# Performance work log

Hardware: AMD Instinct MI355X
Metric: run time of the kernel (lower is better)

## Reference

```python
import jax, jax.numpy as jnp
import numpy as np

B, E, CIN, C, PRE, DME, DEN = 8, 64, 128, 128, 128, 32, 32
N_EDGE_TYPES, N_PATH_TYPES = 10, 20


def leaky(v):
    return jnp.where(v >= 0, v, 0.1 * v)


def setup_inputs() -> dict:
    key = jax.random.key(0)
    ks = jax.random.split(key, 30)
    s = 0.05
    inp = {
        'x': jax.random.normal(ks[0], (B, CIN, E), jnp.float32),
        'y': jax.random.normal(ks[1], (B, CIN, E), jnp.float32),
        'm_bias_mat': jax.random.normal(ks[2], (B, E, E), jnp.float32),
        'edge_mat': jax.random.randint(ks[3], (B, E, E), 0, N_EDGE_TYPES),
        'p_bias_mat': jax.random.normal(ks[4], (B, E, E, E), jnp.float32),
        'path_mat': jax.random.randint(ks[5], (B, E, E, E), 0, N_PATH_TYPES),
        'pre_out': jax.random.normal(ks[6], (B, PRE, E, E), jnp.float32),
        # parameters (conv1d/conv2d k=1 weights squeezed to matrices/vectors)
        'xc1_w': jax.random.normal(ks[7], (C, CIN), jnp.float32) * s,
        'yc1_w': jax.random.normal(ks[8], (C, CIN), jnp.float32) * s,
        'xc2_w': jax.random.normal(ks[9], (C,), jnp.float32) * s,
        'xc2_b': jax.random.normal(ks[10], (1,), jnp.float32) * s,
        'yc2_w': jax.random.normal(ks[11], (C,), jnp.float32) * s,
        'yc2_b': jax.random.normal(ks[12], (1,), jnp.float32) * s,
        'pconv_w': jax.random.normal(ks[13], (DEN,), jnp.float32) * s,
        'econv_w': jax.random.normal(ks[14], (DME,), jnp.float32) * s,
        'conv1_w': jax.random.normal(ks[15], (C, 2 * C + PRE), jnp.float32) * s,
        'conv1_b': jax.random.normal(ks[16], (C,), jnp.float32) * s,
        'conv2_w': jax.random.normal(ks[17], (C, C, 3, 3), jnp.float32) * s,
        'conv2_b': jax.random.normal(ks[18], (C,), jnp.float32) * s,
        'score_w': jax.random.normal(ks[19], (C,), jnp.float32) * s,
        'xlin_w': jax.random.normal(ks[20], (CIN, CIN), jnp.float32) * s,
        'ylin_w': jax.random.normal(ks[21], (CIN, CIN), jnp.float32) * s,
        'edge_table': jax.random.normal(ks[22], (N_EDGE_TYPES, DME), jnp.float32) * s,
        'path_table': jax.random.normal(ks[23], (N_PATH_TYPES, DEN), jnp.float32) * s,
    }
    return inp


def reference(x, y, m_bias_mat, edge_mat, p_bias_mat, path_mat, pre_out,
              xc1_w, yc1_w, xc2_w, xc2_b, yc2_w, yc2_b, pconv_w, econv_w,
              conv1_w, conv1_b, conv2_w, conv2_b, score_w, xlin_w, ylin_w,
              edge_table, path_table):
    # x,y: [B, CIN, E]; M == N == entity_num == E (required by path_fea reshape)
    x_f = jnp.einsum('ci,bim->bcm', xc1_w, x)                    # [B,C,M]
    y_f = jnp.einsum('ci,bin->bcn', yc1_w, y)                    # [B,C,N]
    x_self = jnp.einsum('c,bcm->bm', xc2_w, x_f) + xc2_b         # [B,M]
    y_other = jnp.einsum('c,bcn->bn', yc2_w, y_f) + yc2_b        # [B,N]
    # torch broadcast: [B,1,M] + [B,N,1] -> [B,N,M]
    logist = leaky(x_self[:, None, :] + y_other[:, :, None])     # [B,E,E]

    # ---- per-entity path attention (vectorized over entity axis e) ----
    path_embed = path_table[path_mat]                            # [B,E,M,N,DEN]
    path_logist = leaky(jnp.einsum('bemnd,d->bemn', path_embed, pconv_w))
    local = logist[:, None, :, :] + path_logist + p_bias_mat     # [B,E,M,N]
    A = jax.nn.softmax(local, axis=-1)
    x_ret = leaky(jnp.einsum('bemn,bcn->bcem', A, y_f) + x_f[:, :, None, :])  # [B,C,E,M]
    A2 = jax.nn.softmax(jnp.swapaxes(local, 2, 3), axis=-1)
    y_ret = leaky(jnp.einsum('benm,bcm->bcen', A2, x_f) + y_f[:, :, None, :])  # [B,C,E,N]
    path_fea = jnp.concatenate([x_ret, y_ret], axis=1)           # [B,2C,E,E]

    men = jnp.concatenate([path_fea, pre_out], axis=1)           # [B,2C+PRE,E,E]
    h = leaky(jnp.einsum('oc,bcij->boij', conv1_w, men) + conv1_b[None, :, None, None])
    h = jax.lax.conv_general_dilated(h, conv2_w, (1, 1), 'SAME',
                                     dimension_numbers=('NCHW', 'OIHW', 'NCHW'))
    men2rel = leaky(h + conv2_b[None, :, None, None])            # [B,C,E,E]

    scores = leaky(jnp.einsum('c,bcij->bij', score_w, men2rel))  # [B,E,E]
    edge_logist = leaky(jnp.einsum('bmnd,d->bmn', edge_table[edge_mat], econv_w))
    g = logist + scores + edge_logist + m_bias_mat               # [B,E,E]

    x_lin = jnp.einsum('ij,bjm->bmi', xlin_w, x)                 # [B,M,CIN]
    y_lin = jnp.einsum('ij,bjn->bni', ylin_w, y)                 # [B,N,CIN]
    G = jax.nn.softmax(g, axis=-1)
    out_x = jnp.einsum('bmn,bni->bim', G, y_lin) + x             # residual, [B,CIN,M]
    G2 = jax.nn.softmax(jnp.swapaxes(g, 1, 2), axis=-1)
    out_y = jnp.einsum('bnm,bmi->bin', G2, x_lin) + y            # [B,CIN,N]
    return (out_x, out_y, men2rel)
```

## Files before the change

### kernel.cpp

```cpp
#include <hip/hip_runtime.h>
#include <hip/hip_bf16.h>


typedef unsigned short u16;
typedef unsigned int u32;
typedef short s16x8 __attribute__((ext_vector_type(8)));
typedef float f32x4 __attribute__((ext_vector_type(4)));

__device__ __forceinline__ float b2f(u16 u) { return __uint_as_float(((u32)u) << 16); }
__device__ __forceinline__ u16 f2b(float f) {
    u32 x = __float_as_uint(f);
    u32 r = (x + 0x7fffu + ((x >> 16) & 1u)) >> 16;
    return (u16)r;
}
__device__ __forceinline__ float lk(float v) { return v >= 0.f ? v : 0.1f * v; }
__device__ __forceinline__ s16x8 cvt8(const float* p) {
    float4 a = ((const float4*)p)[0], c = ((const float4*)p)[1];
    s16x8 r;
    r[0] = (short)f2b(a.x); r[1] = (short)f2b(a.y); r[2] = (short)f2b(a.z); r[3] = (short)f2b(a.w);
    r[4] = (short)f2b(c.x); r[5] = (short)f2b(c.y); r[6] = (short)f2b(c.z); r[7] = (short)f2b(c.w);
    return r;
}

__global__ __launch_bounds__(256) void k_prep(const float* __restrict__ w1, const float* __restrict__ w2,
                                              u16* __restrict__ wA1, u16* __restrict__ wA2,
                                              const float* __restrict__ x, const float* __restrict__ y,
                                              const float* __restrict__ xc1, const float* __restrict__ yc1,
                                              const float* __restrict__ xc2w, const float* __restrict__ xc2b,
                                              const float* __restrict__ yc2w, const float* __restrict__ yc2b,
                                              const float* __restrict__ xlw, const float* __restrict__ ylw,
                                              u16* __restrict__ xfb, u16* __restrict__ yfb,
                                              float* __restrict__ xfT, float* __restrict__ yfT,
                                              u16* __restrict__ xlT, u16* __restrict__ ylT,
                                              float* __restrict__ Xs, float* __restrict__ Yo,
                                              const float* __restrict__ pre, u16* __restrict__ menT) {
    int bid = blockIdx.x;
    int t = threadIdx.x;
    if (bid < 768) {
        int idx = bid * 256 + t;
        if (idx < 49152) {
            int e = idx & 7, lane = (idx >> 3) & 63, mtg = (idx >> 9) & 7, kc = idx >> 12;
            int o = mtg * 16 + (lane & 15), c = kc * 32 + ((lane >> 4) << 3) + e;
            wA1[idx] = f2b(w1[o * 384 + c]);
        } else {
            int id2 = idx - 49152;
            if (id2 < 147456) {
                int e = id2 & 7, lane = (id2 >> 3) & 63, mtg = (id2 >> 9) & 7;
                int kc = (id2 >> 12) & 3, tap = id2 >> 14;
                int o = mtg * 16 + (lane & 15), c = kc * 32 + ((lane >> 4) << 3) + e;
                wA2[id2] = f2b(w2[(o * 128 + c) * 9 + tap]);
            }
        }
        return;
    }
    if (bid < 800) {
        int r = bid - 768;
        int b = r >> 2, g4 = r & 3;
        int lane = t & 63, w = t >> 6, l15 = lane & 15, q4 = lane >> 4;
        __shared__ u16 sT[64][136];
        const float* src = (g4 == 0 || g4 == 2) ? x : y;
        const float* wptr = (g4 == 0) ? xc1 : (g4 == 1) ? yc1 : (g4 == 2) ? xlw : ylw;
        {
            int i = t >> 1, m0 = (t & 1) * 32;
            const float4* ps = (const float4*)(src + (b * 128 + i) * 64 + m0);
#pragma unroll
            for (int q = 0; q < 8; ++q) {
                float4 v = ps[q];
                int m = m0 + q * 4;
                sT[m + 0][i] = f2b(v.x); sT[m + 1][i] = f2b(v.y);
                sT[m + 2][i] = f2b(v.z); sT[m + 3][i] = f2b(v.w);
            }
        }
        __syncthreads();
        int m = w * 16 + l15;
        f32x4 acc[8];
#pragma unroll
        for (int mt = 0; mt < 8; ++mt) acc[mt] = (f32x4)(0.f);
#pragma unroll
        for (int kt = 0; kt < 4; ++kt) {
            s16x8 bfr = *(const s16x8*)&sT[m][kt * 32 + q4 * 8];
#pragma unroll
            for (int mt = 0; mt < 8; ++mt) {
                s16x8 af = cvt8(wptr + (mt * 16 + l15) * 128 + kt * 32 + q4 * 8);
                acc[mt] = __builtin_amdgcn_mfma_f32_16x16x32_bf16(af, bfr, acc[mt], 0, 0, 0);
            }
        }
        if (g4 == 0 || g4 == 1) {
            u16* fb = (g4 == 0) ? xfb : yfb;
            float* fT = (g4 == 0) ? xfT : yfT;
            const float* c2w = (g4 == 0) ? xc2w : yc2w;
            const float* c2b = (g4 == 0) ? xc2b : yc2b;
            float* dvec = (g4 == 0) ? Xs : Yo;
            float sp = 0.f;
#pragma unroll
            for (int mt = 0; mt < 8; ++mt) {
                int c0 = mt * 16 + q4 * 4;
                f32x4 a = acc[mt];
                fb[(b * 128 + c0 + 0) * 64 + m] = f2b(a[0]);
                fb[(b * 128 + c0 + 1) * 64 + m] = f2b(a[1]);
                fb[(b * 128 + c0 + 2) * 64 + m] = f2b(a[2]);
                fb[(b * 128 + c0 + 3) * 64 + m] = f2b(a[3]);
                *(float4*)(fT + (b * 64 + m) * 128 + c0) = make_float4(a[0], a[1], a[2], a[3]);
                float4 wv = *(const float4*)(c2w + c0);
                sp += wv.x * a[0] + wv.y * a[1] + wv.z * a[2] + wv.w * a[3];
            }
            sp += __shfl_xor(sp, 16);
            sp += __shfl_xor(sp, 32);
            if (q4 == 0) dvec[b * 64 + m] = sp + c2b[0];
        } else {
            u16* lT = (g4 == 2) ? xlT : ylT;
#pragma unroll
            for (int mt = 0; mt < 8; ++mt) {
                int i0 = mt * 16 + q4 * 4;
                f32x4 a = acc[mt];
                lT[(b * 128 + i0 + 0) * 64 + m] = f2b(a[0]);
                lT[(b * 128 + i0 + 1) * 64 + m] = f2b(a[1]);
                lT[(b * 128 + i0 + 2) * 64 + m] = f2b(a[2]);
                lT[(b * 128 + i0 + 3) * 64 + m] = f2b(a[3]);
            }
        }
        return;
    }
    {
        int r = bid - 800;
        int b = r >> 6, i = r & 63;
        int j = t & 63, pg = t >> 6;
#pragma unroll
        for (int oc = 0; oc < 4; ++oc) {
            int p0 = pg * 32 + oc * 8;
            s16x8 v;
#pragma unroll
            for (int k = 0; k < 8; ++k)
                v[k] = (short)f2b(pre[((b * 128 + p0 + k) * 64 + i) * 64 + j]);
            *(s16x8*)(menT + ((b * 64 + i) * 64 + j) * 384 + 256 + p0) = v;
        }
    }
}

__global__ __launch_bounds__(256) void k_attn(const float* __restrict__ Xs, const float* __restrict__ Yo,
                                              const u16* __restrict__ xfb, const u16* __restrict__ yfb,
                                              const float* __restrict__ xfT, const float* __restrict__ yfT,
                                              const int* __restrict__ path_mat, const float* __restrict__ p_bias,
                                              const float* __restrict__ ptab, const float* __restrict__ pconv,
                                              u16* __restrict__ menT) {
    int b = blockIdx.x >> 6, e = blockIdx.x & 63;
    int t = threadIdx.x;
    int lane = t & 63, w = t >> 6;
    __shared__ float sA[64][68];
    __shared__ u16 Abf[64][72];
    __shared__ u16 E2bf[64][72];
    __shared__ float sRed[256];
    __shared__ float sPdot[20];
    __shared__ float sXv[64], sYv[64];

    if (t < 20) {
        float s = 0.f;
        for (int d = 0; d < 32; ++d) s += ptab[t * 32 + d] * pconv[d];
        sPdot[t] = lk(s);
    } else if (t >= 64 && t < 128) {
        sXv[t - 64] = Xs[b * 64 + t - 64];
    } else if (t >= 128 && t < 192) {
        sYv[t - 128] = Yo[b * 64 + t - 128];
    }
    __syncthreads();

    {
        int m = t >> 2, n0 = (t & 3) * 16;
        int base = (((b * 64 + e) * 64 + m) * 64 + n0);
        const int4* pm4 = (const int4*)(path_mat + base);
        const float4* pb4 = (const float4*)(p_bias + base);
        float yom = sYv[m];
#pragma unroll
        for (int q = 0; q < 4; ++q) {
            int4 pm = pm4[q]; float4 pb = pb4[q];
            int n = n0 + q * 4;
            float4 v;
            v.x = lk(sXv[n + 0] + yom) + sPdot[pm.x] + pb.x;
            v.y = lk(sXv[n + 1] + yom) + sPdot[pm.y] + pb.y;
            v.z = lk(sXv[n + 2] + yom) + sPdot[pm.z] + pb.z;
            v.w = lk(sXv[n + 3] + yom) + sPdot[pm.w] + pb.w;
            *(float4*)&sA[m][n] = v;
        }
    }
    __syncthreads();

    if (t < 128) {
        int r = t >> 1, h = t & 1;
        const float4* rp = (const float4*)&sA[r][h * 32];
        float mx = -1e30f;
#pragma unroll
        for (int k = 0; k < 8; ++k) {
            float4 v = rp[k];
            mx = fmaxf(mx, fmaxf(fmaxf(v.x, v.y), fmaxf(v.z, v.w)));
        }
        mx = fmaxf(mx, __shfl_xor(mx, 1));
        float s = 0.f;
#pragma unroll
        for (int k = 0; k < 8; ++k) {
            float4 v = rp[k];
            s += __expf(v.x - mx) + __expf(v.y - mx) + __expf(v.z - mx) + __expf(v.w - mx);
        }
        s += __shfl_xor(s, 1);
        if (h == 0) { sRed[r] = mx; sRed[64 + r] = 1.f / s; }
    } else {
        int n = (t - 128) >> 1, h = t & 1;
        float mx = -1e30f;
#pragma unroll
        for (int k = 0; k < 32; ++k) mx = fmaxf(mx, sA[h * 32 + k][n]);
        mx = fmaxf(mx, __shfl_xor(mx, 1));
        float s = 0.f;
#pragma unroll
        for (int k = 0; k < 32; ++k) s += __expf(sA[h * 32 + k][n] - mx);
        s += __shfl_xor(s, 1);
        if (h == 0) { sRed[128 + n] = mx; sRed[192 + n] = 1.f / s; }
    }
    __syncthreads();

    {
        int m = t >> 2, q = t & 3;
        float rmax = sRed[m], rinv = sRed[64 + m];
        const float4* rp = (const float4*)&sA[m][q * 16];
#pragma unroll
        for (int g2 = 0; g2 < 2; ++g2) {
            float4 v0 = rp[g2 * 2], v1 = rp[g2 * 2 + 1];
            s16x8 pk;
            pk[0] = (short)f2b(__expf(v0.x - rmax) * rinv);
            pk[1] = (short)f2b(__expf(v0.y - rmax) * rinv);
            pk[2] = (short)f2b(__expf(v0.z - rmax) * rinv);
            pk[3] = (short)f2b(__expf(v0.w - rmax) * rinv);
            pk[4] = (short)f2b(__expf(v1.x - rmax) * rinv);
            pk[5] = (short)f2b(__expf(v1.y - rmax) * rinv);
            pk[6] = (short)f2b(__expf(v1.z - rmax) * rinv);
            pk[7] = (short)f2b(__expf(v1.w - rmax) * rinv);
            *(s16x8*)&Abf[m][q * 16 + g2 * 8] = pk;
        }
    }
    {
        int n = t >> 2, q = t & 3;
        float cmax = sRed[128 + n], cinv = sRed[192 + n];
#pragma unroll
        for (int g2 = 0; g2 < 2; ++g2) {
            s16x8 pk;
#pragma unroll
            for (int k = 0; k < 8; ++k) {
                float v = sA[q * 16 + g2 * 8 + k][n];
                pk[k] = (short)f2b(__expf(v - cmax) * cinv);
            }
            *(s16x8*)&E2bf[n][q * 16 + g2 * 8] = pk;
        }
    }
    __syncthreads();

    int l15 = lane & 15, q4 = lane >> 4;
    {
        f32x4 acc[2][4];
#pragma unroll
        for (int ci = 0; ci < 2; ++ci)
#pragma unroll
            for (int mt = 0; mt < 4; ++mt) acc[ci][mt] = (f32x4)(0.f);
#pragma unroll
        for (int kt = 0; kt < 2; ++kt) {
            s16x8 afr[2];
#pragma unroll
            for (int ci = 0; ci < 2; ++ci) {
                int c = (2 * w + ci) * 16 + l15;
                afr[ci] = *(const s16x8*)(yfb + (b * 128 + c) * 64 + kt * 32 + q4 * 8);
            }
            s16x8 bfr[4];
#pragma unroll
            for (int mt = 0; mt < 4; ++mt)
                bfr[mt] = *(const s16x8*)&Abf[mt * 16 + l15][kt * 32 + q4 * 8];
#pragma unroll
            for (int ci = 0; ci < 2; ++ci)
#pragma unroll
                for (int mt = 0; mt < 4; ++mt)
                    acc[ci][mt] = __builtin_amdgcn_mfma_f32_16x16x32_bf16(afr[ci], bfr[mt], acc[ci][mt], 0, 0, 0);
        }
#pragma unroll
        for (int ci = 0; ci < 2; ++ci) {
            int c0 = (2 * w + ci) * 16 + q4 * 4;
#pragma unroll
            for (int mt = 0; mt < 4; ++mt) {
                int m = mt * 16 + l15;
                float4 res = *(const float4*)(xfT + (b * 64 + m) * 128 + c0);
                f32x4 a = acc[ci][mt];
                u32 lo = (u32)f2b(lk(a[0] + res.x)) | ((u32)f2b(lk(a[1] + res.y)) << 16);
                u32 hi = (u32)f2b(lk(a[2] + res.z)) | ((u32)f2b(lk(a[3] + res.w)) << 16);
                *(uint2*)(menT + ((b * 64 + e) * 64 + m) * 384 + c0) = make_uint2(lo, hi);
            }
        }
    }
    {
        f32x4 acc[2][4];
#pragma unroll
        for (int ci = 0; ci < 2; ++ci)
#pragma unroll
            for (int nt = 0; nt < 4; ++nt) acc[ci][nt] = (f32x4)(0.f);
#pragma unroll
        for (int kt = 0; kt < 2; ++kt) {
            s16x8 afr[2];
#pragma unroll
            for (int ci = 0; ci < 2; ++ci) {
                int c = (2 * w + ci) * 16 + l15;
                afr[ci] = *(const s16x8*)(xfb + (b * 128 + c) * 64 + kt * 32 + q4 * 8);
            }
            s16x8 bfr[4];
#pragma unroll
            for (int nt = 0; nt < 4; ++nt)
                bfr[nt] = *(const s16x8*)&E2bf[nt * 16 + l15][kt * 32 + q4 * 8];
#pragma unroll
            for (int ci = 0; ci < 2; ++ci)
#pragma unroll
                for (int nt = 0; nt < 4; ++nt)
                    acc[ci][nt] = __builtin_amdgcn_mfma_f32_16x16x32_bf16(afr[ci], bfr[nt], acc[ci][nt], 0, 0, 0);
        }
#pragma unroll
        for (int ci = 0; ci < 2; ++ci) {
            int c0 = (2 * w + ci) * 16 + q4 * 4;
#pragma unroll
            for (int nt = 0; nt < 4; ++nt) {
                int n = nt * 16 + l15;
                float4 res = *(const float4*)(yfT + (b * 64 + n) * 128 + c0);
                f32x4 a = acc[ci][nt];
                u32 lo = (u32)f2b(lk(a[0] + res.x)) | ((u32)f2b(lk(a[1] + res.y)) << 16);
                u32 hi = (u32)f2b(lk(a[2] + res.z)) | ((u32)f2b(lk(a[3] + res.w)) << 16);
                *(uint2*)(menT + ((b * 64 + e) * 64 + n) * 384 + 128 + c0) = make_uint2(lo, hi);
            }
        }
    }
}

__global__ __launch_bounds__(256) void k_conv1(const u16* __restrict__ menT, const u16* __restrict__ wA1,
                                               const float* __restrict__ b1, u16* __restrict__ hT) {
    int b = blockIdx.x >> 6, i = blockIdx.x & 63;
    int t = threadIdx.x;
    int lane = t & 63, w = t >> 6, wm = w & 1, wn = w >> 1;
    int l15 = lane & 15, q4 = lane >> 4;

    f32x4 acc[4][2];
#pragma unroll
    for (int mt = 0; mt < 4; ++mt)
#pragma unroll
        for (int nt = 0; nt < 2; ++nt) acc[mt][nt] = (f32x4)(0.f);

    const u16* mrow = menT + (b * 64 + i) * 64 * 384;
    for (int kc = 0; kc < 12; ++kc) {
        s16x8 af[4];
#pragma unroll
        for (int mt = 0; mt < 4; ++mt)
            af[mt] = *(const s16x8*)(wA1 + (((kc * 8 + wm * 4 + mt) * 64 + lane) << 3));
        s16x8 bf[2];
#pragma unroll
        for (int nt = 0; nt < 2; ++nt) {
            int j = (wn * 2 + nt) * 16 + l15;
            bf[nt] = *(const s16x8*)(mrow + j * 384 + kc * 32 + q4 * 8);
        }
#pragma unroll
        for (int mt = 0; mt < 4; ++mt)
#pragma unroll
            for (int nt = 0; nt < 2; ++nt)
                acc[mt][nt] = __builtin_amdgcn_mfma_f32_16x16x32_bf16(af[mt], bf[nt], acc[mt][nt], 0, 0, 0);
    }

#pragma unroll
    for (int mt = 0; mt < 4; ++mt) {
        int o0 = (wm * 4 + mt) * 16 + q4 * 4;
        float4 bb = *(const float4*)(b1 + o0);
#pragma unroll
        for (int nt = 0; nt < 2; ++nt) {
            int j = (wn * 2 + nt) * 16 + l15;
            f32x4 a = acc[mt][nt];
            u32 lo = (u32)f2b(lk(a[0] + bb.x)) | ((u32)f2b(lk(a[1] + bb.y)) << 16);
            u32 hi = (u32)f2b(lk(a[2] + bb.z)) | ((u32)f2b(lk(a[3] + bb.w)) << 16);
            *(uint2*)(hT + ((b * 64 + i) * 64 + j) * 128 + o0) = make_uint2(lo, hi);
        }
    }
}

__global__ __launch_bounds__(256) void k_conv2(const u16* __restrict__ hT, const u16* __restrict__ wA2,
                                               const float* __restrict__ b2, const float* __restrict__ score_w,
                                               const float* __restrict__ Xs, const float* __restrict__ Yo,
                                               const float* __restrict__ etab, const float* __restrict__ econv,
                                               const int* __restrict__ edge_mat, const float* __restrict__ m_bias,
                                               float* __restrict__ m2r, float* __restrict__ g) {
    int b = blockIdx.x >> 6, i = blockIdx.x & 63;
    int t = threadIdx.x;
    int lane = t & 63, w = t >> 6, wm = w & 1, wn = w >> 1;
    int l15 = lane & 15, q4 = lane >> 4;
    __shared__ u16 sB2[3][66][136];
    __shared__ float sSc[2][64];
    __shared__ float sEd[16];

    if (t >= 240 && t < 250) {
        int et = t - 240;
        float s = 0.f;
        for (int d = 0; d < 32; ++d) s += etab[et * 32 + d] * econv[d];
        sEd[et] = lk(s);
    }
#pragma unroll
    for (int q = 0; q < 2; ++q) {
        int u = q * 256 + t;
        if (u < 384) {
            int r = u >> 7, rem = u & 127, hcol = rem >> 6, c2 = rem & 63;
            *(u32*)&sB2[r][hcol ? 65 : 0][c2 * 2] = 0u;
        }
    }
#pragma unroll
    for (int it = 0; it < 12; ++it) {
        int u = it * 256 + t;
        int cg = u & 15, j = (u >> 4) & 63, r = u >> 10;
        int ir = i - 1 + r;
        int4 v = make_int4(0, 0, 0, 0);
        if (ir >= 0 && ir < 64)
            v = *(const int4*)(hT + ((b * 64 + ir) * 64 + j) * 128 + cg * 8);
        *(int4*)&sB2[r][j + 1][cg * 8] = v;
    }
    __syncthreads();

    f32x4 acc[4][2];
#pragma unroll
    for (int mt = 0; mt < 4; ++mt)
#pragma unroll
        for (int nt = 0; nt < 2; ++nt) acc[mt][nt] = (f32x4)(0.f);

    for (int kc = 0; kc < 4; ++kc) {
#pragma unroll
        for (int tap = 0; tap < 9; ++tap) {
            int di = tap / 3, dj = tap % 3;
            s16x8 af[4];
#pragma unroll
            for (int mt = 0; mt < 4; ++mt)
                af[mt] = *(const s16x8*)(wA2 + ((((tap * 4 + kc) * 8 + wm * 4 + mt) * 64 + lane) << 3));
#pragma unroll
            for (int nt = 0; nt < 2; ++nt) {
                int jin = wn * 32 + nt * 16 + l15 + dj;
                s16x8 bf = *(const s16x8*)(&sB2[di][jin][kc * 32 + q4 * 8]);
#pragma unroll
                for (int mt = 0; mt < 4; ++mt)
                    acc[mt][nt] = __builtin_amdgcn_mfma_f32_16x16x32_bf16(af[mt], bf, acc[mt][nt], 0, 0, 0);
            }
        }
    }

    float part[2] = {0.f, 0.f};
#pragma unroll
    for (int mt = 0; mt < 4; ++mt) {
        int o0 = wm * 64 + mt * 16 + q4 * 4;
        float4 bb = *(const float4*)(b2 + o0);
        float4 sw = *(const float4*)(score_w + o0);
#pragma unroll
        for (int nt = 0; nt < 2; ++nt) {
            int j = wn * 32 + nt * 16 + l15;
            f32x4 a = acc[mt][nt];
            float v0 = lk(a[0] + bb.x), v1 = lk(a[1] + bb.y);
            float v2 = lk(a[2] + bb.z), v3 = lk(a[3] + bb.w);
            float* dst = m2r + ((b * 128 + o0) * 64 + i) * 64 + j;
            dst[0] = v0; dst[4096] = v1; dst[8192] = v2; dst[12288] = v3;
            part[nt] += sw.x * v0 + sw.y * v1 + sw.z * v2 + sw.w * v3;
        }
    }
#pragma unroll
    for (int nt = 0; nt < 2; ++nt) {
        float p = part[nt];
        p += __shfl_xor(p, 16);
        p += __shfl_xor(p, 32);
        if (q4 == 0) sSc[wm][wn * 32 + nt * 16 + l15] = p;
    }
    __syncthreads();
    if (t < 64) {
        float s = sSc[0][t] + sSc[1][t];
        int gi = (b * 64 + i) * 64 + t;
        float L = lk(Xs[b * 64 + t] + Yo[b * 64 + i]);
        g[gi] = L + sEd[edge_mat[gi]] + m_bias[gi] + lk(s);
    }
}

__global__ __launch_bounds__(256) void k_gout(const float* __restrict__ g,
                                              const u16* __restrict__ xlT, const u16* __restrict__ ylT,
                                              const float* __restrict__ x, const float* __restrict__ y,
                                              float* __restrict__ out) {
    int b = blockIdx.x >> 1, which = blockIdx.x & 1;
    int t = threadIdx.x;
    int lane = t & 63, w = t >> 6, l15 = lane & 15, q4 = lane >> 4;
    __shared__ float sG[64][68];
    __shared__ u16 Gbf[64][72];
    __shared__ float sRed[128];

#pragma unroll
    for (int r = 0; r < 16; ++r) {
        int idx = r * 256 + t;
        sG[idx >> 6][idx & 63] = g[b * 4096 + idx];
    }
    __syncthreads();

    if (which == 0) {
        if (t < 128) {
            int r = t >> 1, h = t & 1;
            const float4* rp = (const float4*)&sG[r][h * 32];
            float mx = -1e30f;
#pragma unroll
            for (int k = 0; k < 8; ++k) {
                float4 v = rp[k];
                mx = fmaxf(mx, fmaxf(fmaxf(v.x, v.y), fmaxf(v.z, v.w)));
            }
            mx = fmaxf(mx, __shfl_xor(mx, 1));
            float s = 0.f;
#pragma unroll
            for (int k = 0; k < 8; ++k) {
                float4 v = rp[k];
                s += __expf(v.x - mx) + __expf(v.y - mx) + __expf(v.z - mx) + __expf(v.w - mx);
            }
            s += __shfl_xor(s, 1);
            if (h == 0) { sRed[r] = mx; sRed[64 + r] = 1.f / s; }
        }
        __syncthreads();
        int m = t >> 2, q = t & 3;
        float rmax = sRed[m], rinv = sRed[64 + m];
        const float4* rp = (const float4*)&sG[m][q * 16];
#pragma unroll
        for (int g2 = 0; g2 < 2; ++g2) {
            float4 v0 = rp[g2 * 2], v1 = rp[g2 * 2 + 1];
            s16x8 pk;
            pk[0] = (short)f2b(__expf(v0.x - rmax) * rinv);
            pk[1] = (short)f2b(__expf(v0.y - rmax) * rinv);
            pk[2] = (short)f2b(__expf(v0.z - rmax) * rinv);
            pk[3] = (short)f2b(__expf(v0.w - rmax) * rinv);
            pk[4] = (short)f2b(__expf(v1.x - rmax) * rinv);
            pk[5] = (short)f2b(__expf(v1.y - rmax) * rinv);
            pk[6] = (short)f2b(__expf(v1.z - rmax) * rinv);
            pk[7] = (short)f2b(__expf(v1.w - rmax) * rinv);
            *(s16x8*)&Gbf[m][q * 16 + g2 * 8] = pk;
        }
    } else {
        if (t < 128) {
            int n = t >> 1, h = t & 1;
            float mx = -1e30f;
#pragma unroll
            for (int k = 0; k < 32; ++k) mx = fmaxf(mx, sG[h * 32 + k][n]);
            mx = fmaxf(mx, __shfl_xor(mx, 1));
            float s = 0.f;
#pragma unroll
            for (int k = 0; k < 32; ++k) s += __expf(sG[h * 32 + k][n] - mx);
            s += __shfl_xor(s, 1);
            if (h == 0) { sRed[n] = mx; sRed[64 + n] = 1.f / s; }
        }
        __syncthreads();
        int n = t >> 2, q = t & 3;
        float cmax = sRed[n], cinv = sRed[64 + n];
#pragma unroll
        for (int g2 = 0; g2 < 2; ++g2) {
            s16x8 pk;
#pragma unroll
            for (int k = 0; k < 8; ++k) {
                float v = sG[q * 16 + g2 * 8 + k][n];
                pk[k] = (short)f2b(__expf(v - cmax) * cinv);
            }
            *(s16x8*)&Gbf[n][q * 16 + g2 * 8] = pk;
        }
    }
    __syncthreads();

    const u16* lT = which ? xlT : ylT;
    const float* res = which ? y : x;
    int off = which ? 65536 : 0;
    int mcol = w * 16 + l15;
    f32x4 acc[8];
#pragma unroll
    for (int mt = 0; mt < 8; ++mt) acc[mt] = (f32x4)(0.f);
#pragma unroll
    for (int kt = 0; kt < 2; ++kt) {
        s16x8 bfr = *(const s16x8*)&Gbf[mcol][kt * 32 + q4 * 8];
#pragma unroll
        for (int mt = 0; mt < 8; ++mt) {
            s16x8 af = *(const s16x8*)(lT + (b * 128 + mt * 16 + l15) * 64 + kt * 32 + q4 * 8);
            acc[mt] = __builtin_amdgcn_mfma_f32_16x16x32_bf16(af, bfr, acc[mt], 0, 0, 0);
        }
    }
#pragma unroll
    for (int mt = 0; mt < 8; ++mt) {
        int i0 = mt * 16 + q4 * 4;
        f32x4 a = acc[mt];
#pragma unroll
        for (int r = 0; r < 4; ++r) {
            int ad = (b * 128 + i0 + r) * 64 + mcol;
            out[off + ad] = a[r] + res[ad];
        }
    }
}

extern "C" void kernel_launch(void* const* d_in, const int* in_sizes, int n_in,
                              void* d_out, int out_size, void* d_ws, size_t ws_size,
                              hipStream_t stream) {
    const float* x = (const float*)d_in[0];
    const float* y = (const float*)d_in[1];
    const float* m_bias = (const float*)d_in[2];
    const int* edge_mat = (const int*)d_in[3];
    const float* p_bias = (const float*)d_in[4];
    const int* path_mat = (const int*)d_in[5];
    const float* pre = (const float*)d_in[6];
    const float* xc1 = (const float*)d_in[7];
    const float* yc1 = (const float*)d_in[8];
    const float* xc2w = (const float*)d_in[9];
    const float* xc2b = (const float*)d_in[10];
    const float* yc2w = (const float*)d_in[11];
    const float* yc2b = (const float*)d_in[12];
    const float* pconv = (const float*)d_in[13];
    const float* econv = (const float*)d_in[14];
    const float* w1 = (const float*)d_in[15];
    const float* b1 = (const float*)d_in[16];
    const float* w2 = (const float*)d_in[17];
    const float* b2 = (const float*)d_in[18];
    const float* score_w = (const float*)d_in[19];
    const float* xlw = (const float*)d_in[20];
    const float* ylw = (const float*)d_in[21];
    const float* etab = (const float*)d_in[22];
    const float* ptab = (const float*)d_in[23];

    float* Xs = (float*)d_ws;
    float* Yo = Xs + 512;
    float* g = Yo + 512;
    float* xfT = g + 32768;
    float* yfT = xfT + 65536;
    u16* wA1 = (u16*)(yfT + 65536);
    u16* wA2 = wA1 + 49152;
    u16* xfb = wA2 + 147456;
    u16* yfb = xfb + 65536;
    u16* xlT = yfb + 65536;
    u16* ylT = xlT + 65536;
    u16* menT = ylT + 65536;
    u16* hT = menT + 12582912;

    float* out = (float*)d_out;
    float* out_m2r = out + 131072;

    hipLaunchKernelGGL(k_prep, dim3(1312), dim3(256), 0, stream, w1, w2, wA1, wA2,
                       x, y, xc1, yc1, xc2w, xc2b, yc2w, yc2b, xlw, ylw,
                       xfb, yfb, xfT, yfT, xlT, ylT, Xs, Yo, pre, menT);
    hipLaunchKernelGGL(k_attn, dim3(512), dim3(256), 0, stream, Xs, Yo, xfb, yfb, xfT, yfT,
                       path_mat, p_bias, ptab, pconv, menT);
    hipLaunchKernelGGL(k_conv1, dim3(512), dim3(256), 0, stream, menT, wA1, b1, hT);
    hipLaunchKernelGGL(k_conv2, dim3(512), dim3(256), 0, stream, hT, wA2, b2, score_w,
                       Xs, Yo, etab, econv, edge_mat, m_bias, out_m2r, g);
    hipLaunchKernelGGL(k_gout, dim3(16), dim3(256), 0, stream, g, xlT, ylT, x, y, out);
}
```

Baseline: 190.5 us.

## Fuse conv1 into attention kernel keeping path features in shared memory

Merges the conv1 1x1 GEMM into the attention kernel. The x/y path features stay in LDS (aliased over the score buffer) instead of going through a 384-wide global menT buffer, and only the pre_out part is read from a narrower preT buffer. The softmaxes are also reworked to compute exp once, using a global max per row, and to derive column sums by rescaling, which removes repeated exp work. This cuts a kernel launch and a large global round trip at the cost of more LDS and registers per block, and the global-max trick carries some risk of underflow.

```diff
diff --git a/kernel.cpp b/kernel.cpp
--- a/kernel.cpp
+++ b/kernel.cpp
@@ -33,7 +33,7 @@
                                               float* __restrict__ xfT, float* __restrict__ yfT,
                                               u16* __restrict__ xlT, u16* __restrict__ ylT,
                                               float* __restrict__ Xs, float* __restrict__ Yo,
-                                              const float* __restrict__ pre, u16* __restrict__ menT) {
+                                              const float* __restrict__ pre, u16* __restrict__ preT) {
     int bid = blockIdx.x;
     int t = threadIdx.x;
     if (bid < 768) {
@@ -132,26 +132,31 @@
 #pragma unroll
             for (int k = 0; k < 8; ++k)
                 v[k] = (short)f2b(pre[((b * 128 + p0 + k) * 64 + i) * 64 + j]);
-            *(s16x8*)(menT + ((b * 64 + i) * 64 + j) * 384 + 256 + p0) = v;
+            *(s16x8*)(preT + ((b * 64 + i) * 64 + j) * 128 + p0) = v;
         }
     }
 }
 
-__global__ __launch_bounds__(256) void k_attn(const float* __restrict__ Xs, const float* __restrict__ Yo,
-                                              const u16* __restrict__ xfb, const u16* __restrict__ yfb,
-                                              const float* __restrict__ xfT, const float* __restrict__ yfT,
-                                              const int* __restrict__ path_mat, const float* __restrict__ p_bias,
-                                              const float* __restrict__ ptab, const float* __restrict__ pconv,
-                                              u16* __restrict__ menT) {
+__global__ __launch_bounds__(256) void k_attnc(const float* __restrict__ Xs, const float* __restrict__ Yo,
+                                               const u16* __restrict__ xfb, const u16* __restrict__ yfb,
+                                               const float* __restrict__ xfT, const float* __restrict__ yfT,
+                                               const int* __restrict__ path_mat, const float* __restrict__ p_bias,
+                                               const float* __restrict__ ptab, const float* __restrict__ pconv,
+                                               const u16* __restrict__ preT, const u16* __restrict__ wA1,
+                                               const float* __restrict__ b1, u16* __restrict__ hT) {
     int b = blockIdx.x >> 6, e = blockIdx.x & 63;
     int t = threadIdx.x;
     int lane = t & 63, w = t >> 6;
-    __shared__ float sA[64][68];
+    __shared__ __align__(16) char smem0[64 * 264 * 2];
+    float* sAf = (float*)smem0;
+    u16* sMen = (u16*)smem0;
     __shared__ u16 Abf[64][72];
     __shared__ u16 E2bf[64][72];
     __shared__ float sRed[256];
     __shared__ float sPdot[20];
     __shared__ float sXv[64], sYv[64];
+
+    int tr = t >> 2, tq = t & 3, tn0 = tq * 16;
 
     if (t < 20) {
         float s = 0.f;
@@ -165,88 +170,93 @@
     __syncthreads();
 
     {
-        int m = t >> 2, n0 = (t & 3) * 16;
-        int base = (((b * 64 + e) * 64 + m) * 64 + n0);
+        int base = (((b * 64 + e) * 64 + tr) * 64 + tn0);
         const int4* pm4 = (const int4*)(path_mat + base);
         const float4* pb4 = (const float4*)(p_bias + base);
-        float yom = sYv[m];
-#pragma unroll
-        for (int q = 0; q < 4; ++q) {
-            int4 pm = pm4[q]; float4 pb = pb4[q];
-            int n = n0 + q * 4;
+        float yom = sYv[tr];
+        float mx = -1e30f;
+#pragma unroll
+        for (int q2 = 0; q2 < 4; ++q2) {
+            int4 pm = pm4[q2]; float4 pb = pb4[q2];
+            int n = tn0 + q2 * 4;
             float4 v;
             v.x = lk(sXv[n + 0] + yom) + sPdot[pm.x] + pb.x;
             v.y = lk(sXv[n + 1] + yom) + sPdot[pm.y] + pb.y;
             v.z = lk(sXv[n + 2] + yom) + sPdot[pm.z] + pb.z;
             v.w = lk(sXv[n + 3] + yom) + sPdot[pm.w] + pb.w;
-            *(float4*)&sA[m][n] = v;
-        }
-    }
-    __syncthreads();
-
-    if (t < 128) {
-        int r = t >> 1, h = t & 1;
-        const float4* rp = (const float4*)&sA[r][h * 32];
-        float mx = -1e30f;
-#pragma unroll
-        for (int k = 0; k < 8; ++k) {
-            float4 v = rp[k];
+            *(float4*)&sAf[tr * 68 + n] = v;
             mx = fmaxf(mx, fmaxf(fmaxf(v.x, v.y), fmaxf(v.z, v.w)));
         }
         mx = fmaxf(mx, __shfl_xor(mx, 1));
+        mx = fmaxf(mx, __shfl_xor(mx, 2));
+        if (tq == 0) sRed[tr] = mx;
+    }
+    __syncthreads();
+
+    if (t < 64) {
+        float rm = sRed[t];
+        float M = rm;
+#pragma unroll
+        for (int off = 1; off < 64; off <<= 1) M = fmaxf(M, __shfl_xor(M, off));
+        sRed[128 + t] = __expf(rm - M);
+    }
+    {
+        float rmax = sRed[tr];
+        float4* rp = (float4*)&sAf[tr * 68 + tn0];
         float s = 0.f;
 #pragma unroll
-        for (int k = 0; k < 8; ++k) {
-            float4 v = rp[k];
-            s += __expf(v.x - mx) + __expf(v.y - mx) + __expf(v.z - mx) + __expf(v.w - mx);
+        for (int q2 = 0; q2 < 4; ++q2) {
+            float4 v = rp[q2];
+            float4 ev;
+            ev.x = __expf(v.x - rmax); ev.y = __expf(v.y - rmax);
+            ev.z = __expf(v.z - rmax); ev.w = __expf(v.w - rmax);
+            s += ev.x + ev.y + ev.z + ev.w;
+            rp[q2] = ev;
         }
         s += __shfl_xor(s, 1);
-        if (h == 0) { sRed[r] = mx; sRed[64 + r] = 1.f / s; }
-    } else {
-        int n = (t - 128) >> 1, h = t & 1;
-        float mx = -1e30f;
-#pragma unroll
-        for (int k = 0; k < 32; ++k) mx = fmaxf(mx, sA[h * 32 + k][n]);
-        mx = fmaxf(mx, __shfl_xor(mx, 1));
-        float s = 0.f;
-#pragma unroll
-        for (int k = 0; k < 32; ++k) s += __expf(sA[h * 32 + k][n] - mx);
-        s += __shfl_xor(s, 1);
-        if (h == 0) { sRed[128 + n] = mx; sRed[192 + n] = 1.f / s; }
-    }
-    __syncthreads();
-
-    {
-        int m = t >> 2, q = t & 3;
-        float rmax = sRed[m], rinv = sRed[64 + m];
-        const float4* rp = (const float4*)&sA[m][q * 16];
+        s += __shfl_xor(s, 2);
+        if (tq == 0) sRed[64 + tr] = 1.f / s;
+    }
+    __syncthreads();
+
+    {
+        float cs = 0.f;
+#pragma unroll
+        for (int k = 0; k < 16; ++k) {
+            int mm = tn0 + k;
+            cs += sAf[mm * 68 + tr] * sRed[128 + mm];
+        }
+        cs += __shfl_xor(cs, 1);
+        cs += __shfl_xor(cs, 2);
+        if (tq == 0) sRed[192 + tr] = 1.f / cs;
+    }
+    __syncthreads();
+
+    {
+        float rinv = sRed[64 + tr];
+        const float4* rp = (const float4*)&sAf[tr * 68 + tn0];
 #pragma unroll
         for (int g2 = 0; g2 < 2; ++g2) {
             float4 v0 = rp[g2 * 2], v1 = rp[g2 * 2 + 1];
             s16x8 pk;
-            pk[0] = (short)f2b(__expf(v0.x - rmax) * rinv);
-            pk[1] = (short)f2b(__expf(v0.y - rmax) * rinv);
-            pk[2] = (short)f2b(__expf(v0.z - rmax) * rinv);
-            pk[3] = (short)f2b(__expf(v0.w - rmax) * rinv);
-            pk[4] = (short)f2b(__expf(v1.x - rmax) * rinv);
-            pk[5] = (short)f2b(__expf(v1.y - rmax) * rinv);
-            pk[6] = (short)f2b(__expf(v1.z - rmax) * rinv);
-            pk[7] = (short)f2b(__expf(v1.w - rmax) * rinv);
-            *(s16x8*)&Abf[m][q * 16 + g2 * 8] = pk;
-        }
-    }
-    {
-        int n = t >> 2, q = t & 3;
-        float cmax = sRed[128 + n], cinv = sRed[192 + n];
+            pk[0] = (short)f2b(v0.x * rinv); pk[1] = (short)f2b(v0.y * rinv);
+            pk[2] = (short)f2b(v0.z * rinv); pk[3] = (short)f2b(v0.w * rinv);
+            pk[4] = (short)f2b(v1.x * rinv); pk[5] = (short)f2b(v1.y * rinv);
+            pk[6] = (short)f2b(v1.z * rinv); pk[7] = (short)f2b(v1.w * rinv);
+            *(s16x8*)&Abf[tr][tn0 + g2 * 8] = pk;
+        }
+    }
+    {
+        float cinv = sRed[192 + tr];
 #pragma unroll
         for (int g2 = 0; g2 < 2; ++g2) {
             s16x8 pk;
 #pragma unroll
             for (int k = 0; k < 8; ++k) {
-                float v = sA[q * 16 + g2 * 8 + k][n];
-                pk[k] = (short)f2b(__expf(v - cmax) * cinv);
-            }
-            *(s16x8*)&E2bf[n][q * 16 + g2 * 8] = pk;
+                int mm = tn0 + g2 * 8 + k;
+                pk[k] = (short)f2b(sAf[mm * 68 + tr] * sRed[128 + mm] * cinv);
+            }
+            *(s16x8*)&E2bf[tr][tn0 + g2 * 8] = pk;
         }
     }
     __syncthreads();
@@ -286,7 +296,7 @@
                 f32x4 a = acc[ci][mt];
                 u32 lo = (u32)f2b(lk(a[0] + res.x)) | ((u32)f2b(lk(a[1] + res.y)) << 16);
                 u32 hi = (u32)f2b(lk(a[2] + res.z)) | ((u32)f2b(lk(a[3] + res.w)) << 16);
-                *(uint2*)(menT + ((b * 64 + e) * 64 + m) * 384 + c0) = make_uint2(lo, hi);
+                *(uint2*)&sMen[m * 264 + c0] = make_uint2(lo, hi);
             }
         }
     }
@@ -324,55 +334,50 @@
                 f32x4 a = acc[ci][nt];
                 u32 lo = (u32)f2b(lk(a[0] + res.x)) | ((u32)f2b(lk(a[1] + res.y)) << 16);
                 u32 hi = (u32)f2b(lk(a[2] + res.z)) | ((u32)f2b(lk(a[3] + res.w)) << 16);
-                *(uint2*)(menT + ((b * 64 + e) * 64 + n) * 384 + 128 + c0) = make_uint2(lo, hi);
-            }
-        }
-    }
-}
-
-__global__ __launch_bounds__(256) void k_conv1(const u16* __restrict__ menT, const u16* __restrict__ wA1,
-                                               const float* __restrict__ b1, u16* __restrict__ hT) {
-    int b = blockIdx.x >> 6, i = blockIdx.x & 63;
-    int t = threadIdx.x;
-    int lane = t & 63, w = t >> 6, wm = w & 1, wn = w >> 1;
-    int l15 = lane & 15, q4 = lane >> 4;
-
-    f32x4 acc[4][2];
-#pragma unroll
-    for (int mt = 0; mt < 4; ++mt)
-#pragma unroll
-        for (int nt = 0; nt < 2; ++nt) acc[mt][nt] = (f32x4)(0.f);
-
-    const u16* mrow = menT + (b * 64 + i) * 64 * 384;
-    for (int kc = 0; kc < 12; ++kc) {
-        s16x8 af[4];
+                *(uint2*)&sMen[n * 264 + 128 + c0] = make_uint2(lo, hi);
+            }
+        }
+    }
+    __syncthreads();
+
+    {
+        int wm = w & 1, wn = w >> 1;
+        f32x4 acc[4][2];
 #pragma unroll
         for (int mt = 0; mt < 4; ++mt)
-            af[mt] = *(const s16x8*)(wA1 + (((kc * 8 + wm * 4 + mt) * 64 + lane) << 3));
-        s16x8 bf[2];
-#pragma unroll
-        for (int nt = 0; nt < 2; ++nt) {
-            int j = (wn * 2 + nt) * 16 + l15;
-            bf[nt] = *(const s16x8*)(mrow + j * 384 + kc * 32 + q4 * 8);
-        }
-#pragma unroll
-        for (int mt = 0; mt < 4; ++mt)
-#pragma unroll
-            for (int nt = 0; nt < 2; ++nt)
-                acc[mt][nt] = __builtin_amdgcn_mfma_f32_16x16x32_bf16(af[mt], bf[nt], acc[mt][nt], 0, 0, 0);
-    }
-
-#pragma unroll
-    for (int mt = 0; mt < 4; ++mt) {
-        int o0 = (wm * 4 + mt) * 16 + q4 * 4;
-        float4 bb = *(const float4*)(b1 + o0);
-#pragma unroll
-        for (int nt = 0; nt < 2; ++nt) {
-            int j = (wn * 2 + nt) * 16 + l15;
-            f32x4 a = acc[mt][nt];
-            u32 lo = (u32)f2b(lk(a[0] + bb.x)) | ((u32)f2b(lk(a[1] + bb.y)) << 16);
-            u32 hi = (u32)f2b(lk(a[2] + bb.z)) | ((u32)f2b(lk(a[3] + bb.w)) << 16);
-            *(uint2*)(hT + ((b * 64 + i) * 64 + j) * 128 + o0) = make_uint2(lo, hi);
+#pragma unroll
+            for (int nt = 0; nt < 2; ++nt) acc[mt][nt] = (f32x4)(0.f);
+        const u16* prow = preT + (b * 64 + e) * 64 * 128;
+        for (int kc = 0; kc < 12; ++kc) {
+            s16x8 af[4];
+#pragma unroll
+            for (int mt = 0; mt < 4; ++mt)
+                af[mt] = *(const s16x8*)(wA1 + (((kc * 8 + wm * 4 + mt) * 64 + lane) << 3));
+            s16x8 bf[2];
+#pragma unroll
+            for (int nt = 0; nt < 2; ++nt) {
+                int j = (wn * 2 + nt) * 16 + l15;
+                bf[nt] = (kc < 8) ? *(const s16x8*)&sMen[j * 264 + kc * 32 + q4 * 8]
+                                  : *(const s16x8*)(prow + j * 128 + (kc - 8) * 32 + q4 * 8);
+            }
+#pragma unroll
+            for (int mt = 0; mt < 4; ++mt)
+#pragma unroll
+                for (int nt = 0; nt < 2; ++nt)
+                    acc[mt][nt] = __builtin_amdgcn_mfma_f32_16x16x32_bf16(af[mt], bf[nt], acc[mt][nt], 0, 0, 0);
+        }
+#pragma unroll
+        for (int mt = 0; mt < 4; ++mt) {
+            int o0 = (wm * 4 + mt) * 16 + q4 * 4;
+            float4 bb = *(const float4*)(b1 + o0);
+#pragma unroll
+            for (int nt = 0; nt < 2; ++nt) {
+                int j = (wn * 2 + nt) * 16 + l15;
+                f32x4 a = acc[mt][nt];
+                u32 lo = (u32)f2b(lk(a[0] + bb.x)) | ((u32)f2b(lk(a[1] + bb.y)) << 16);
+                u32 hi = (u32)f2b(lk(a[2] + bb.z)) | ((u32)f2b(lk(a[3] + bb.w)) << 16);
+                *(uint2*)(hT + ((b * 64 + e) * 64 + j) * 128 + o0) = make_uint2(lo, hi);
+            }
         }
     }
 }
@@ -484,78 +489,85 @@
     int lane = t & 63, w = t >> 6, l15 = lane & 15, q4 = lane >> 4;
     __shared__ float sG[64][68];
     __shared__ u16 Gbf[64][72];
-    __shared__ float sRed[128];
-
-#pragma unroll
-    for (int r = 0; r < 16; ++r) {
-        int idx = r * 256 + t;
-        sG[idx >> 6][idx & 63] = g[b * 4096 + idx];
+    __shared__ float sRed[256];
+
+    int tr = t >> 2, tq = t & 3, tn0 = tq * 16;
+
+    {
+        const float4* gp = (const float4*)(g + b * 4096 + tr * 64 + tn0);
+        float mx = -1e30f;
+#pragma unroll
+        for (int q2 = 0; q2 < 4; ++q2) {
+            float4 v = gp[q2];
+            *(float4*)&sG[tr][tn0 + q2 * 4] = v;
+            mx = fmaxf(mx, fmaxf(fmaxf(v.x, v.y), fmaxf(v.z, v.w)));
+        }
+        mx = fmaxf(mx, __shfl_xor(mx, 1));
+        mx = fmaxf(mx, __shfl_xor(mx, 2));
+        if (tq == 0) sRed[tr] = mx;
+    }
+    __syncthreads();
+    if (t < 64) {
+        float rm = sRed[t], M = rm;
+#pragma unroll
+        for (int off = 1; off < 64; off <<= 1) M = fmaxf(M, __shfl_xor(M, off));
+        sRed[128 + t] = __expf(rm - M);
+    }
+    {
+        float rmax = sRed[tr];
+        float4* rp = (float4*)&sG[tr][tn0];
+        float s = 0.f;
+#pragma unroll
+        for (int q2 = 0; q2 < 4; ++q2) {
+            float4 v = rp[q2];
+            float4 ev;
+            ev.x = __expf(v.x - rmax); ev.y = __expf(v.y - rmax);
+            ev.z = __expf(v.z - rmax); ev.w = __expf(v.w - rmax);
+            s += ev.x + ev.y + ev.z + ev.w;
+            rp[q2] = ev;
+        }
+        s += __shfl_xor(s, 1);
+        s += __shfl_xor(s, 2);
+        if (tq == 0) sRed[64 + tr] = 1.f / s;
     }
     __syncthreads();
 
     if (which == 0) {
-        if (t < 128) {
-            int r = t >> 1, h = t & 1;
-            const float4* rp = (const float4*)&sG[r][h * 32];
-            float mx = -1e30f;
-#pragma unroll
-            for (int k = 0; k < 8; ++k) {
-                float4 v = rp[k];
-                mx = fmaxf(mx, fmaxf(fmaxf(v.x, v.y), fmaxf(v.z, v.w)));
-            }
-            mx = fmaxf(mx, __shfl_xor(mx, 1));
-            float s = 0.f;
-#pragma unroll
-            for (int k = 0; k < 8; ++k) {
-                float4 v = rp[k];
-                s += __expf(v.x - mx) + __expf(v.y - mx) + __expf(v.z - mx) + __expf(v.w - mx);
-            }
-            s += __shfl_xor(s, 1);
-            if (h == 0) { sRed[r] = mx; sRed[64 + r] = 1.f / s; }
-        }
-        __syncthreads();
-        int m = t >> 2, q = t & 3;
-        float rmax = sRed[m], rinv = sRed[64 + m];
-        const float4* rp = (const float4*)&sG[m][q * 16];
+        float rinv = sRed[64 + tr];
+        const float4* rp = (const float4*)&sG[tr][tn0];
 #pragma unroll
         for (int g2 = 0; g2 < 2; ++g2) {
             float4 v0 = rp[g2 * 2], v1 = rp[g2 * 2 + 1];
             s16x8 pk;
-            pk[0] = (short)f2b(__expf(v0.x - rmax) * rinv);
-            pk[1] = (short)f2b(__expf(v0.y - rmax) * rinv);
-            pk[2] = (short)f2b(__expf(v0.z - rmax) * rinv);
-            pk[3] = (short)f2b(__expf(v0.w - rmax) * rinv);
-            pk[4] = (short)f2b(__expf(v1.x - rmax) * rinv);
-            pk[5] = (short)f2b(__expf(v1.y - rmax) * rinv);
-            pk[6] = (short)f2b(__expf(v1.z - rmax) * rinv);
-            pk[7] = (short)f2b(__expf(v1.w - rmax) * rinv);
-            *(s16x8*)&Gbf[m][q * 16 + g2 * 8] = pk;
+            pk[0] = (short)f2b(v0.x * rinv); pk[1] = (short)f2b(v0.y * rinv);
+            pk[2] = (short)f2b(v0.z * rinv); pk[3] = (short)f2b(v0.w * rinv);
+            pk[4] = (short)f2b(v1.x * rinv); pk[5] = (short)f2b(v1.y * rinv);
+            pk[6] = (short)f2b(v1.z * rinv); pk[7] = (short)f2b(v1.w * rinv);
+            *(s16x8*)&Gbf[tr][tn0 + g2 * 8] = pk;
         }
     } else {
-        if (t < 128) {
-            int n = t >> 1, h = t & 1;
-            float mx = -1e30f;
-#pragma unroll
-            for (int k = 0; k < 32; ++k) mx = fmaxf(mx, sG[h * 32 + k][n]);
-            mx = fmaxf(mx, __shfl_xor(mx, 1));
-            float s = 0.f;
-#pragma unroll
-            for (int k = 0; k < 32; ++k) s += __expf(sG[h * 32 + k][n] - mx);
-            s += __shfl_xor(s, 1);
-            if (h == 0) { sRed[n] = mx; sRed[64 + n] = 1.f / s; }
-        }
-        __syncthreads();
-        int n = t >> 2, q = t & 3;
-        float cmax = sRed[n], cinv = sRed[64 + n];
+        float cs = 0.f;
+#pragma unroll
+        for (int k = 0; k < 16; ++k) {
+            int mm = tn0 + k;
+            cs += sG[mm][tr] * sRed[128 + mm];
+        }
+        cs += __shfl_xor(cs, 1);
+        cs += __shfl_xor(cs, 2);
+        if (tq == 0) sRed[192 + tr] = 1.f / cs;
+    }
+    __syncthreads();
+    if (which == 1) {
+        float cinv = sRed[192 + tr];
 #pragma unroll
         for (int g2 = 0; g2 < 2; ++g2) {
             s16x8 pk;
 #pragma unroll
             for (int k = 0; k < 8; ++k) {
-                float v = sG[q * 16 + g2 * 8 + k][n];
-                pk[k] = (short)f2b(__expf(v - cmax) * cinv);
-            }
-            *(s16x8*)&Gbf[n][q * 16 + g2 * 8] = pk;
+                int mm = tn0 + g2 * 8 + k;
+                pk[k] = (short)f2b(sG[mm][tr] * sRed[128 + mm] * cinv);
+            }
+            *(s16x8*)&Gbf[tr][tn0 + g2 * 8] = pk;
         }
     }
     __syncthreads();
@@ -627,18 +639,17 @@
     u16* yfb = xfb + 65536;
     u16* xlT = yfb + 65536;
     u16* ylT = xlT + 65536;
-    u16* menT = ylT + 65536;
-    u16* hT = menT + 12582912;
+    u16* preT = ylT + 65536;
+    u16* hT = preT + 4194304;
 
     float* out = (float*)d_out;
     float* out_m2r = out + 131072;
 
     hipLaunchKernelGGL(k_prep, dim3(1312), dim3(256), 0, stream, w1, w2, wA1, wA2,
                        x, y, xc1, yc1, xc2w, xc2b, yc2w, yc2b, xlw, ylw,
-                       xfb, yfb, xfT, yfT, xlT, ylT, Xs, Yo, pre, menT);
-    hipLaunchKernelGGL(k_attn, dim3(512), dim3(256), 0, stream, Xs, Yo, xfb, yfb, xfT, yfT,
-                       path_mat, p_bias, ptab, pconv, menT);
-    hipLaunchKernelGGL(k_conv1, dim3(512), dim3(256), 0, stream, menT, wA1, b1, hT);
+                       xfb, yfb, xfT, yfT, xlT, ylT, Xs, Yo, pre, preT);
+    hipLaunchKernelGGL(k_attnc, dim3(512), dim3(256), 0, stream, Xs, Yo, xfb, yfb, xfT, yfT,
+                       path_mat, p_bias, ptab, pconv, preT, wA1, b1, hT);
     hipLaunchKernelGGL(k_conv2, dim3(512), dim3(256), 0, stream, hT, wA2, b2, score_w,
                        Xs, Yo, etab, econv, edge_mat, m_bias, out_m2r, g);
     hipLaunchKernelGGL(k_gout, dim3(16), dim3(256), 0, stream, g, xlT, ylT, x, y, out);
```

Measured after the change: 179.6 us. 1.06x faster.
